# Performance work log

Hardware: AMD Instinct MI355X
Metric: run time of the kernel (lower is better)

Reference implementation:

```python
import jax, jax.numpy as jnp
import numpy as np

EPS = 1e-6
HID = 2048; N_HEADS = 16; Q_LORA = 768; KV_LORA = 512
ROPE_D = 64; NOPE_D = 128; V_D = 128
IDX_H = 32; IDX_D = 128; IDX_TOPK = 512
N_EXP = 8; TOPK = 4; N_GROUP = 4; TOPK_GROUP = 2
MOE_I = 512; SHARED_I = 512; ROUTED_SCALE = 2.5
T = 1024
NEG = -1e30


def _rms(x, w, eps=EPS):
    x = x.astype(jnp.float32)
    return x * jax.lax.rsqrt(jnp.mean(x * x, axis=-1, keepdims=True) + eps) * w


def _ln(x, w, b, eps=EPS):
    x = x.astype(jnp.float32)
    m = jnp.mean(x, axis=-1, keepdims=True)
    v = jnp.mean((x - m) ** 2, axis=-1, keepdims=True)
    return (x - m) * jax.lax.rsqrt(v + eps) * w + b


def _rope_cs(positions, dim):
    inv = 1.0 / (10000.0 ** (jnp.arange(0, dim, 2, dtype=jnp.float32) / dim))
    f = positions.astype(jnp.float32)[:, None] * inv[None, :]  # [T, dim/2]
    return jnp.cos(f), jnp.sin(f)


def _rope(x, cos, sin):
    # neox-style rotate-half over last dim
    d = x.shape[-1] // 2
    x1, x2 = x[..., :d], x[..., d:]
    while cos.ndim < x.ndim:
        cos, sin = cos[:, None], sin[:, None]
    return jnp.concatenate([x1 * cos - x2 * sin, x2 * cos + x1 * sin], axis=-1)


def setup_inputs() -> dict:
    key = jax.random.key(0)
    ks = iter(jax.random.split(key, 32))
    w = lambda *s: jax.random.normal(next(ks), s, jnp.float32) * 0.02
    inp = {
        'positions': jnp.arange(T, dtype=jnp.int32),
        'hidden_states': jax.random.normal(next(ks), (T, HID), jnp.float32),
        'residual': jax.random.normal(next(ks), (T, HID), jnp.float32),
        'w_input_ln': jnp.ones((HID,), jnp.float32),
        'w_post_ln': jnp.ones((HID,), jnp.float32),
        'w_step1': w(Q_LORA + KV_LORA + ROPE_D + IDX_D + IDX_H, HID),
        'w_q_a_ln': jnp.ones((Q_LORA,), jnp.float32),
        'w_kv_a_ln': jnp.ones((KV_LORA,), jnp.float32),
        'idx_k_ln_w': jnp.ones((IDX_D,), jnp.float32),
        'idx_k_ln_b': jnp.zeros((IDX_D,), jnp.float32),
        'w_step3': w(IDX_H * IDX_D + N_HEADS * (NOPE_D + ROPE_D), Q_LORA),
        'W_UK_T': w(N_HEADS, NOPE_D, KV_LORA),
        'W_UV': w(N_HEADS, KV_LORA, V_D),
        'w_o': w(HID, N_HEADS * V_D),
        'gate_w': w(N_EXP, HID),
        'gate_bias': jnp.zeros((N_EXP,), jnp.float32),
        'shared_gate_up': w(2 * SHARED_I, HID),
        'shared_down': w(HID, SHARED_I),
        'exp_gate_up': w(N_EXP, 2 * MOE_I, HID),
        'exp_down': w(N_EXP, HID, MOE_I),
    }
    return inp


def reference(positions, hidden_states, residual, w_input_ln, w_post_ln, w_step1,
              w_q_a_ln, w_kv_a_ln, idx_k_ln_w, idx_k_ln_b, w_step3, W_UK_T, W_UV,
              w_o, gate_w, gate_bias, shared_gate_up, shared_down, exp_gate_up, exp_down):
    Tn = hidden_states.shape[0]
    rows = jnp.arange(Tn)
    # (allreduce is identity at tp=1) + residual add + RMSNorm
    res = hidden_states.astype(jnp.float32) + residual.astype(jnp.float32)
    h = _rms(res, w_input_ln)
    # ---- Step 1: fused qkv_a + indexer_wk + indexer_weights_proj GEMM ----
    s1 = h @ w_step1.T
    o0 = 0
    q_c = s1[:, o0:o0 + Q_LORA]; o0 += Q_LORA
    kv_c = s1[:, o0:o0 + KV_LORA]; o0 += KV_LORA
    k_pe = s1[:, o0:o0 + ROPE_D]; o0 += ROPE_D
    idx_k = s1[:, o0:o0 + IDX_D]; o0 += IDX_D
    idx_w_raw = s1[:, o0:o0 + IDX_H]
    cos, sin = _rope_cs(positions, ROPE_D)
    # fused_norm_rope: norms + rope on k_pe / indexer-k
    q_c = _rms(q_c, w_q_a_ln)
    kv_c = _rms(kv_c, w_kv_a_ln)
    k_pe = _rope(k_pe, cos, sin)
    idx_k = _ln(idx_k, idx_k_ln_w, idx_k_ln_b)
    idx_k = jnp.concatenate([_rope(idx_k[:, :ROPE_D], cos, sin), idx_k[:, ROPE_D:]], axis=-1)
    # ---- Step 3: fused indexer_wq_b + q_b_proj GEMM ----
    s3 = q_c @ w_step3.T
    idx_q = s3[:, :IDX_H * IDX_D].reshape(Tn, IDX_H, IDX_D)
    q = s3[:, IDX_H * IDX_D:].reshape(Tn, N_HEADS, NOPE_D + ROPE_D)
    q_nope, q_pe = q[..., :NOPE_D], q[..., NOPE_D:]
    # absorb W_UK: [T,H,nope] x [H,nope,kv_lora] -> [T,H,kv_lora]
    ql_nope = jnp.einsum('thn,hnk->thk', q_nope, W_UK_T)
    q_pe = _rope(q_pe, cos, sin)
    idx_q = jnp.concatenate([_rope(idx_q[..., :ROPE_D], cos, sin), idx_q[..., ROPE_D:]], axis=-1)
    idx_q = idx_q * (IDX_D ** -0.5)            # indexer softmax scale
    idx_w = idx_w_raw * (IDX_H ** -0.5)        # per-head weights scale
    # ---- sparse attention indexer: relu(q.k) head-weighted sum, causal top-k ----
    il = jnp.einsum('thd,sd->ths', idx_q, idx_k)          # [T,Hi,S]
    iscores = jnp.einsum('ths,th->ts', jax.nn.relu(il), idx_w)
    causal = positions[:, None] >= positions[None, :]
    iscores = jnp.where(causal, iscores, NEG)
    topk_idx = jax.lax.top_k(iscores, IDX_TOPK)[1]        # [T, IDX_TOPK]
    tmask = jnp.zeros((Tn, Tn), bool).at[rows[:, None], topk_idx].set(True)
    mask = causal & tmask
    # ---- MLA MQA attention in latent space ----
    mqa_q = jnp.concatenate([ql_nope, jnp.broadcast_to(q_pe, (Tn, N_HEADS, ROPE_D))], axis=-1)
    kv = jnp.concatenate([kv_c, k_pe], axis=-1)           # [S, kv_lora+rope]
    att = jnp.einsum('thd,sd->hts', mqa_q, kv) * ((NOPE_D + ROPE_D) ** -0.5)
    att = jnp.where(mask[None], att, NEG)
    p = jax.nn.softmax(att, axis=-1)
    o = jnp.einsum('hts,sk->thk', p, kv_c)                # [T,H,kv_lora]
    o = jnp.einsum('thk,hkv->thv', o, W_UV).reshape(Tn, N_HEADS * V_D)
    attn_out = o @ w_o.T
    # add + RMSNorm
    res2 = attn_out + res
    h2 = _rms(res2, w_post_ln)
    # ---- MoE: DeepSeekV3 sigmoid grouped routing + shared experts ----
    glog = h2 @ gate_w.T
    sg = jax.nn.sigmoid(glog)
    sc = sg + gate_bias
    gsz = N_EXP // N_GROUP
    grp = sc.reshape(Tn, N_GROUP, gsz)
    grp_score = jax.lax.top_k(grp, min(2, gsz))[0].sum(-1)
    gidx = jax.lax.top_k(grp_score, TOPK_GROUP)[1]
    gmask = jnp.zeros((Tn, N_GROUP), bool).at[rows[:, None], gidx].set(True)
    emask = jnp.repeat(gmask, gsz, axis=1)
    sc_m = jnp.where(emask, sc, NEG)
    _, tid = jax.lax.top_k(sc_m, TOPK)
    tw = jnp.take_along_axis(sg, tid, axis=1)
    tw = tw / (tw.sum(-1, keepdims=True) + 1e-20) * ROUTED_SCALE
    comb = jnp.zeros((Tn, N_EXP), jnp.float32).at[rows[:, None], tid].set(tw)
    # routed experts (dense masked combine as reference for grouped-GEMM dispatch)
    gu = jnp.einsum('th,eih->tei', h2, exp_gate_up)       # [T,E,2I]
    act = jax.nn.silu(gu[..., :MOE_I]) * gu[..., MOE_I:]
    routed_e = jnp.einsum('tei,ehi->teh', act, exp_down)  # [T,E,H]
    routed = jnp.einsum('te,teh->th', comb, routed_e)
    # shared experts
    gus = h2 @ shared_gate_up.T
    shared = (jax.nn.silu(gus[:, :SHARED_I]) * gus[:, SHARED_I:]) @ shared_down.T
    out = shared + routed
    return out, res2
```

## Files before the change

### kernel.cpp

```cpp
#include <hip/hip_runtime.h>
#include <math.h>

static constexpr int TT  = 1024;
static constexpr int HID = 2048;
static constexpr int NH  = 16;
static constexpr int QL  = 768;
static constexpr int KVL = 512;
static constexpr int RD  = 64;
static constexpr int IH  = 32;
static constexpr int ID  = 128;
static constexpr int S1W = QL + KVL + RD + ID + IH;
static constexpr int S3W = IH*ID + NH*(128+RD);

#define SCALE_ATT 0.07216878364870323f
#define SC_IDXQ   0.08838834764831845f
#define SC_IDXW   0.17677669529663687f
#define NEGR      -1e30f
#define NEGL      -3.0e38f

typedef __bf16 bf16x8 __attribute__((ext_vector_type(8)));
typedef float  f32x4  __attribute__((ext_vector_type(4)));

#define GLD_LDS16(g, l) __builtin_amdgcn_global_load_lds( \
    (const __attribute__((address_space(1))) void*)(g),   \
    (__attribute__((address_space(3))) void*)(l), 16, 0, 0)

__device__ __forceinline__ unsigned short f2b(float x) {
  union { float f; unsigned u; } v; v.f = x;
  unsigned r = v.u + 0x7FFFu + ((v.u >> 16) & 1u);
  return (unsigned short)(r >> 16);
}
__device__ __forceinline__ float b2f(unsigned short u) {
  union { unsigned u; float f; } v; v.u = ((unsigned)u) << 16;
  return v.f;
}

__device__ __forceinline__ float blk_sum256(float v, float* s) {
  #pragma unroll
  for (int o = 32; o > 0; o >>= 1) v += __shfl_down(v, o, 64);
  __syncthreads();
  if ((threadIdx.x & 63) == 0) s[threadIdx.x >> 6] = v;
  __syncthreads();
  return s[0] + s[1] + s[2] + s[3];
}

__global__ __launch_bounds__(256) void k_prelude(const float* __restrict__ hs,
                                                 const float* __restrict__ rsd,
                                                 const float* __restrict__ w,
                                                 float* __restrict__ res,
                                                 unsigned short* __restrict__ hb) {
  int t = blockIdx.x;
  __shared__ float scr[4];
  float vals[8]; float ss = 0.f;
  #pragma unroll
  for (int r = 0; r < 8; r++) {
    int d = threadIdx.x + 256*r;
    float v = hs[(size_t)t*HID + d] + rsd[(size_t)t*HID + d];
    vals[r] = v; res[(size_t)t*HID + d] = v; ss = fmaf(v, v, ss);
  }
  ss = blk_sum256(ss, scr);
  float inv = 1.f/sqrtf(ss/(float)HID + 1e-6f);
  #pragma unroll
  for (int r = 0; r < 8; r++) {
    int d = threadIdx.x + 256*r;
    hb[(size_t)t*HID + d] = f2b(vals[r]*inv*w[d]);
  }
}

__global__ __launch_bounds__(256) void k_res2(const float* __restrict__ attn1,
                                              const float* __restrict__ attn2,
                                              const float* __restrict__ res,
                                              const float* __restrict__ w,
                                              float* __restrict__ res2_out,
                                              float* __restrict__ h2,
                                              unsigned short* __restrict__ h2b) {
  int t = blockIdx.x;
  __shared__ float scr[4];
  float vals[8]; float ss = 0.f;
  #pragma unroll
  for (int r = 0; r < 8; r++) {
    int d = threadIdx.x + 256*r;
    float v = attn1[(size_t)t*HID + d] + attn2[(size_t)t*HID + d] + res[(size_t)t*HID + d];
    vals[r] = v; res2_out[(size_t)t*HID + d] = v; ss = fmaf(v, v, ss);
  }
  ss = blk_sum256(ss, scr);
  float inv = 1.f/sqrtf(ss/(float)HID + 1e-6f);
  #pragma unroll
  for (int r = 0; r < 8; r++) {
    int d = threadIdx.x + 256*r;
    float o = vals[r]*inv*w[d];
    h2[(size_t)t*HID + d] = o;
    h2b[(size_t)t*HID + d] = f2b(o);
  }
}

__global__ void k_ropecs(const int* __restrict__ pos, float* __restrict__ cosb, float* __restrict__ sinb) {
  int i = blockIdx.x*256 + threadIdx.x;
  if (i >= TT*32) return;
  int t = i >> 5, k = i & 31;
  double inv = pow(10000.0, -((double)(2*k))/64.0);
  double f = (double)pos[t] * inv;
  cosb[i] = (float)cos(f);
  sinb[i] = (float)sin(f);
}

__global__ void k_f2b(const float* __restrict__ s, unsigned short* __restrict__ d,
                      long long n, long long ntot) {
  long long stride = (long long)gridDim.x * 1024;
  for (long long i = ((long long)blockIdx.x*256 + threadIdx.x)*4; i < ntot; i += stride) {
    float x0, x1, x2, x3;
    if (i + 3 < n) { float4 v = *(const float4*)(s + i); x0=v.x; x1=v.y; x2=v.z; x3=v.w; }
    else {
      x0 = (i   < n) ? s[i]   : 0.f; x1 = (i+1 < n) ? s[i+1] : 0.f;
      x2 = (i+2 < n) ? s[i+2] : 0.f; x3 = (i+3 < n) ? s[i+3] : 0.f;
    }
    ushort4 o; o.x=f2b(x0); o.y=f2b(x1); o.z=f2b(x2); o.w=f2b(x3);
    *(ushort4*)(d + i) = o;
  }
}

__global__ void k_f2b4(const float* __restrict__ s0, unsigned short* __restrict__ d0, long long n0,
                       const float* __restrict__ s1, unsigned short* __restrict__ d1, long long n1,
                       const float* __restrict__ s2, unsigned short* __restrict__ d2, long long n2,
                       const float* __restrict__ s3, unsigned short* __restrict__ d3, long long n3) {
  long long ntot = n0 + n1 + n2 + n3;
  long long stride = (long long)gridDim.x * 1024;
  for (long long i = ((long long)blockIdx.x*256 + threadIdx.x)*4; i < ntot; i += stride) {
    const float* s; unsigned short* d; long long j = i;
    if (j < n0) { s = s0; d = d0; }
    else { j -= n0;
      if (j < n1) { s = s1; d = d1; }
      else { j -= n1;
        if (j < n2) { s = s2; d = d2; }
        else { j -= n2; s = s3; d = d3; } } }
    float4 v = *(const float4*)(s + j);
    ushort4 o; o.x=f2b(v.x); o.y=f2b(v.y); o.z=f2b(v.z); o.w=f2b(v.w);
    *(ushort4*)(d + j) = o;
  }
}

__global__ __launch_bounds__(256) void k_tconvb(const float* __restrict__ src,
                                                unsigned short* __restrict__ dst,
                                                int R, int C) {
  src += (size_t)blockIdx.z * R * C;
  dst += (size_t)blockIdx.z * R * C;
  __shared__ float tile[32][33];
  int c0 = blockIdx.x * 32, r0 = blockIdx.y * 32;
  int tx = threadIdx.x & 31, ty = threadIdx.x >> 5;
  #pragma unroll
  for (int i = 0; i < 4; i++) {
    int r = r0 + ty + i*8;
    tile[ty + i*8][tx] = src[(size_t)r*C + c0 + tx];
  }
  __syncthreads();
  #pragma unroll
  for (int i = 0; i < 4; i++) {
    int c = c0 + ty + i*8;
    dst[(size_t)c*R + r0 + tx] = f2b(tile[tx][ty + i*8]);
  }
}

template<int OUT, bool ILV, int MOE>
__global__ __launch_bounds__(256) void k_mgemm(
    const unsigned short* __restrict__ A, int lda, long long sA,
    const unsigned short* __restrict__ B, int ldb, long long sB,
    void* __restrict__ Cv, int ldc, long long sC,
    int N, int K, float alpha, int cskip, int ktri,
    int nseg, long long segA, long long segB,
    const float* __restrict__ comb,
    const int* __restrict__ cntp, const int* __restrict__ tokp) {
  const int row0 = blockIdx.y * 128;
  const int col0 = blockIdx.x * 128;
  if (cskip >= 0 && col0 > row0 + cskip) return;
  const int zb = blockIdx.z;
  int cnt = 0; long long off = 0;
  if (MOE) {
    cnt = cntp[zb];
    for (int e = 0; e < zb; e++) off += cntp[e];
    if (row0 >= cnt) return;
  }
  __shared__ __align__(16) unsigned short As[128*64];
  __shared__ __align__(16) unsigned short Bs[128*64];
  const int tid  = threadIdx.x;
  const int wave = tid >> 6, lane = tid & 63;
  const int wm = wave >> 1, wn = wave & 1;
  A += (size_t)zb * (size_t)sA;
  B += (size_t)zb * (size_t)sB;
  if (MOE == 2) A += off * (long long)lda;

  int tki[4];
  if (MOE == 1) {
    #pragma unroll
    for (int it = 0; it < 4; it++) {
      int r = (wave*64 + it*256 + lane) >> 3;
      tki[it] = tokp[zb*1024 + row0 + r];
    }
  }

  f32x4 acc[4][4] = {};
  const int l15 = lane & 15, l4 = lane >> 4;
  const int sx = l15 & 7;
  const int Kend = (ktri && K > row0 + 128) ? (row0 + 128) : K;

  for (int seg = 0; seg < nseg; seg++) {
    const unsigned short* Ab = A + (size_t)seg * segA;
    const unsigned short* Bb = B + (size_t)seg * segB;
    for (int k0 = 0; k0 < Kend; k0 += 64) {
      __syncthreads();
      #pragma unroll
      for (int it = 0; it < 4; it++) {
        int base = wave*64 + it*256;
        int sidx = base + lane;
        int r = sidx >> 3, s = sidx & 7;
        int s_src = s ^ (r & 7);
        const unsigned short* ga;
        if (MOE == 1) ga = Ab + (size_t)tki[it]*lda + k0 + s_src*8;
        else          ga = Ab + (size_t)(row0 + r)*lda + k0 + s_src*8;
        GLD_LDS16(ga, As + base*8);
        int rt = col0 + r;
        int srow = ILV ? ((rt >> 1) + (rt & 1)*512) : rt;
        const unsigned short* gb = Bb + (size_t)srow*ldb + k0 + s_src*8;
        GLD_LDS16(gb, Bs + base*8);
      }
      __syncthreads();
      #pragma unroll
      for (int kc = 0; kc < 2; kc++) {
        const int sl = ((kc*4 + l4) ^ sx) << 3;
        bf16x8 fa[4], fb[4];
        #pragma unroll
        for (int mf = 0; mf < 4; mf++)
          fa[mf] = *(const bf16x8*)&As[(wm*64 + mf*16 + l15)*64 + sl];
        #pragma unroll
        for (int nf = 0; nf < 4; nf++)
          fb[nf] = *(const bf16x8*)&Bs[(wn*64 + nf*16 + l15)*64 + sl];
        #pragma unroll
        for (int mf = 0; mf < 4; mf++)
          #pragma unroll
          for (int nf = 0; nf < 4; nf++)
            acc[mf][nf] = __builtin_amdgcn_mfma_f32_16x16x32_bf16(fa[mf], fb[nf], acc[mf][nf], 0, 0, 0);
      }
    }
  }

  #pragma unroll
  for (int mf = 0; mf < 4; mf++) {
    #pragma unroll
    for (int nf = 0; nf < 4; nf++) {
      int n = col0 + wn*64 + nf*16 + l15;
      #pragma unroll
      for (int r = 0; r < 4; r++) {
        int m = row0 + wm*64 + mf*16 + l4*4 + r;
        float v = acc[mf][nf][r] * alpha;
        if (OUT == 2) {
          float p = __shfl_xor(v, 1, 64);
          if ((l15 & 1) == 0) {
            bool ok = true;
            long long mrow = m;
            float w;
            if (MOE == 1) {
              ok = (m < cnt); mrow = off + m;
              int tok = tokp[zb*1024 + m];
              w = (zb < 8) ? comb[tok*8 + zb] : 1.f;
            } else {
              w = (zb < 8) ? comb[m*8 + zb] : 1.f;
            }
            if (ok) {
              float rres = v/(1.f + expf(-v)) * p * w;
              ((unsigned short*)Cv)[(size_t)zb*sC + (size_t)mrow*ldc + (n >> 1)] = f2b(rres);
            }
          }
        } else if (n < N) {
          bool ok = true;
          long long mrow = m;
          if (MOE == 2) { ok = (m < cnt); mrow = off + m; }
          if (ok) {
            size_t idx = (size_t)mrow*ldc + n;
            if (OUT == 1) ((unsigned short*)Cv)[(size_t)zb*sC + idx] = f2b(v);
            else          ((float*)Cv)[(size_t)zb*sC + idx] = v;
          }
        }
      }
    }
  }
}

__global__ __launch_bounds__(256) void k_post1(const float* __restrict__ s1a,
    const float* __restrict__ s1b,
    const float* __restrict__ wq, const float* __restrict__ wkv,
    const float* __restrict__ lnw, const float* __restrict__ lnb,
    const float* __restrict__ cosb, const float* __restrict__ sinb,
    unsigned short* __restrict__ qcb, float* __restrict__ kvc, float* __restrict__ kpe,
    float* __restrict__ idxk, float* __restrict__ idxw) {
  int t = blockIdx.x, tid = threadIdx.x;
  __shared__ float rowb[S1W];
  __shared__ float scr[4];
  __shared__ float yb[128];
  for (int d = tid; d < S1W; d += 256)
    rowb[d] = s1a[(size_t)t*S1W + d] + s1b[(size_t)t*S1W + d];
  __syncthreads();
  float ss = 0.f;
  for (int d = tid; d < QL; d += 256) { float v = rowb[d]; ss = fmaf(v,v,ss); }
  ss = blk_sum256(ss, scr);
  float inv = 1.f/sqrtf(ss/(float)QL + 1e-6f);
  for (int d = tid; d < QL; d += 256) qcb[(size_t)t*QL + d] = f2b(rowb[d]*inv*wq[d]);
  ss = 0.f;
  for (int d = tid; d < KVL; d += 256) { float v = rowb[QL+d]; ss = fmaf(v,v,ss); }
  ss = blk_sum256(ss, scr);
  inv = 1.f/sqrtf(ss/(float)KVL + 1e-6f);
  for (int d = tid; d < KVL; d += 256) kvc[(size_t)t*KVL + d] = rowb[QL+d]*inv*wkv[d];
  float sm = (tid < 128) ? rowb[1344 + tid] : 0.f;
  float tot = blk_sum256(sm, scr);
  float mean = tot / 128.f;
  float vs = 0.f;
  if (tid < 128) { float v = rowb[1344+tid] - mean; vs = v*v; }
  vs = blk_sum256(vs, scr);
  float ivn = 1.f/sqrtf(vs/128.f + 1e-6f);
  if (tid < 128) yb[tid] = (rowb[1344+tid]-mean)*ivn*lnw[tid] + lnb[tid];
  __syncthreads();
  if (tid < 32) {
    float c = cosb[t*32 + tid], s = sinb[t*32 + tid];
    idxk[(size_t)t*ID + tid]      = yb[tid]*c - yb[32+tid]*s;
    idxk[(size_t)t*ID + 32 + tid] = yb[32+tid]*c + yb[tid]*s;
    float x1 = rowb[1280+tid], x2 = rowb[1312+tid];
    kpe[(size_t)t*RD + tid]      = x1*c - x2*s;
    kpe[(size_t)t*RD + 32 + tid] = x2*c + x1*s;
    idxw[(size_t)t*IH + tid] = rowb[1472+tid] * SC_IDXW;
  } else if (tid >= 64 && tid < 128) {
    idxk[(size_t)t*ID + tid] = yb[tid];
  }
}

__global__ __launch_bounds__(256) void k_post3b(const float* __restrict__ s3,
                                                const float* __restrict__ cosb,
                                                const float* __restrict__ sinb,
                                                unsigned short* __restrict__ s3b) {
  int t = blockIdx.x, tid = threadIdx.x;
  const float* row = s3 + (size_t)t*S3W;
  __shared__ float buf[S3W];
  __shared__ float cs[32], sn[32];
  if (tid < 32) { cs[tid] = cosb[t*32+tid]; sn[tid] = sinb[t*32+tid]; }
  for (int d = tid; d < S3W; d += 256) buf[d] = row[d];
  __syncthreads();
  for (int p = tid; p < 1024; p += 256) {
    int h = p >> 5, d = p & 31;
    float c = cs[d], s = sn[d];
    float x1 = buf[h*ID + d], x2 = buf[h*ID + 32 + d];
    buf[h*ID + d]      = (x1*c - x2*s) * SC_IDXQ;
    buf[h*ID + 32 + d] = (x2*c + x1*s) * SC_IDXQ;
  }
  for (int p = tid; p < 2048; p += 256) {
    int h = p >> 6, d = 64 + (p & 63);
    buf[h*ID + d] *= SC_IDXQ;
  }
  for (int p = tid; p < 512; p += 256) {
    int h = p >> 5, d = p & 31;
    float c = cs[d], s = sn[d];
    int base = IH*ID + h*192 + 128;
    float x1 = buf[base + d], x2 = buf[base + 32 + d];
    buf[base + d]      = x1*c - x2*s;
    buf[base + 32 + d] = x2*c + x1*s;
  }
  __syncthreads();
  unsigned short* orow = s3b + (size_t)t*S3W;
  for (int g = tid*4; g < S3W; g += 1024) {
    ushort4 o;
    o.x = f2b(buf[g]); o.y = f2b(buf[g+1]); o.z = f2b(buf[g+2]); o.w = f2b(buf[g+3]);
    *(ushort4*)(orow + g) = o;
  }
}

__global__ void k_qpe(const unsigned short* __restrict__ s3b, unsigned short* __restrict__ qm) {
  int i = blockIdx.x*256 + threadIdx.x;
  int t = i >> 10, r = i & 1023;
  int h = r >> 6, j = r & 63;
  float v = b2f(s3b[(size_t)t*S3W + IH*ID + h*192 + 128 + j]) * SCALE_ATT;
  qm[(size_t)t*9216 + h*576 + 512 + j] = f2b(v);
}

__global__ void k_kvb(const float* __restrict__ kvc, const float* __restrict__ kpe,
                      unsigned short* __restrict__ kvb) {
  int i = blockIdx.x*256 + threadIdx.x;
  int s = i / 576, d = i - s*576;
  float v = (d < 512) ? kvc[(size_t)s*KVL + d] : kpe[(size_t)s*RD + (d - 512)];
  kvb[i] = f2b(v);
}

__global__ __launch_bounds__(256) void k_ired(const float* __restrict__ il,
                                              const float* __restrict__ idxw,
                                              float* __restrict__ isc,
                                              int first, int last, int h0) {
  int tr = blockIdx.x;
  int t = 512 + tr;
  int s0 = threadIdx.x * 4;
  float4 acc;
  if (first) acc = make_float4(0.f, 0.f, 0.f, 0.f);
  else       acc = *(float4*)(isc + (size_t)tr*TT + s0);
  #pragma unroll
  for (int hh = 0; hh < 8; hh++) {
    float w = idxw[t*IH + h0 + hh];
    float4 v = *(const float4*)(il + (size_t)hh*524288 + (size_t)tr*1024 + s0);
    acc.x += fmaxf(v.x, 0.f) * w;
    acc.y += fmaxf(v.y, 0.f) * w;
    acc.z += fmaxf(v.z, 0.f) * w;
    acc.w += fmaxf(v.w, 0.f) * w;
  }
  if (last) {
    if (s0     > t) acc.x = NEGR;
    if (s0 + 1 > t) acc.y = NEGR;
    if (s0 + 2 > t) acc.z = NEGR;
    if (s0 + 3 > t) acc.w = NEGR;
  }
  *(float4*)(isc + (size_t)tr*TT + s0) = acc;
}

__global__ __launch_bounds__(512) void k_topk(const float* __restrict__ isc,
                                              unsigned char* __restrict__ mask) {
  int t = 512 + blockIdx.x;
  const float* row = isc + (size_t)blockIdx.x * TT;
  __shared__ unsigned long long keys[1024];
  int tid = threadIdx.x;
  for (int i = tid; i < 1024; i += 512) {
    float v = row[i];
    unsigned int b = __float_as_uint(v);
    unsigned int u = (b & 0x80000000u) ? ~b : (b | 0x80000000u);
    keys[i] = ((unsigned long long)u << 32) | (unsigned int)(1023 - i);
  }
  __syncthreads();
  for (int k = 2; k <= 1024; k <<= 1) {
    for (int j = k >> 1; j > 0; j >>= 1) {
      int i = ((tid & ~(j - 1)) << 1) | (tid & (j - 1));
      int l = i | j;
      unsigned long long a = keys[i], b = keys[l];
      bool up = ((i & k) == 0);
      if ((a < b) == up) { keys[i] = b; keys[l] = a; }
      __syncthreads();
    }
  }
  unsigned char* mrow = mask + (size_t)t * TT;
  for (int p = tid; p < 1024; p += 512) {
    int s = 1023 - (int)(keys[p] & 0xFFFFFFFFu);
    mrow[s] = (p < 512) ? (unsigned char)1 : (unsigned char)0;
  }
}

__global__ __launch_bounds__(256) void k_psoft(unsigned short* __restrict__ pb,
                                               const unsigned char* __restrict__ mask) {
  int b = blockIdx.x;
  int t = b & 1023, h = b >> 10;
  unsigned short* row = pb + ((size_t)h << 20) + ((size_t)t << 10);
  int tid = threadIdx.x;
  __shared__ float scr[4];
  int s0 = tid * 4;
  int rub = ((t >> 7) + 1) << 7;
  bool act = (s0 < rub);
  float v0 = 0.f, v1 = 0.f, v2 = 0.f, v3 = 0.f;
  bool m0 = false, m1 = false, m2 = false, m3 = false;
  if (act) {
    ushort4 raw = *(const ushort4*)(row + s0);
    v0 = b2f(raw.x); v1 = b2f(raw.y); v2 = b2f(raw.z); v3 = b2f(raw.w);
    if (t < 512) {
      m0 = (s0 <= t); m1 = (s0+1 <= t); m2 = (s0+2 <= t); m3 = (s0+3 <= t);
    } else {
      uchar4 mk = *(const uchar4*)(mask + (size_t)t*TT + s0);
      m0 = (s0 <= t) && mk.x; m1 = (s0+1 <= t) && mk.y;
      m2 = (s0+2 <= t) && mk.z; m3 = (s0+3 <= t) && mk.w;
    }
  }
  float mx = NEGL;
  if (m0) mx = v0;
  if (m1) mx = fmaxf(mx, v1);
  if (m2) mx = fmaxf(mx, v2);
  if (m3) mx = fmaxf(mx, v3);
  #pragma unroll
  for (int o = 32; o > 0; o >>= 1) mx = fmaxf(mx, __shfl_down(mx, o, 64));
  __syncthreads();
  if ((tid & 63) == 0) scr[tid >> 6] = mx;
  __syncthreads();
  mx = fmaxf(fmaxf(scr[0], scr[1]), fmaxf(scr[2], scr[3]));
  float p0 = m0 ? expf(v0 - mx) : 0.f;
  float p1 = m1 ? expf(v1 - mx) : 0.f;
  float p2 = m2 ? expf(v2 - mx) : 0.f;
  float p3 = m3 ? expf(v3 - mx) : 0.f;
  float sum = blk_sum256((p0+p1)+(p2+p3), scr);
  float inv = 1.f / sum;
  if (act) {
    ushort4 o;
    o.x = f2b(p0*inv); o.y = f2b(p1*inv); o.z = f2b(p2*inv); o.w = f2b(p3*inv);
    *(ushort4*)(row + s0) = o;
  }
}

__global__ __launch_bounds__(256) void k_gate(const float* __restrict__ h2,
                                              const float* __restrict__ gw,
                                              const float* __restrict__ gb,
                                              float* __restrict__ comb) {
  int t = blockIdx.x, tid = threadIdx.x;
  int e = tid >> 5, lane = tid & 31;
  __shared__ float gl[8];
  float p = 0.f;
  for (int d = lane; d < HID; d += 32) p = fmaf(h2[(size_t)t*HID+d], gw[(size_t)e*HID+d], p);
  #pragma unroll
  for (int o = 16; o > 0; o >>= 1) p += __shfl_down(p, o, 32);
  if (lane == 0) gl[e] = p;
  __syncthreads();
  if (tid == 0) {
    float sg[8], sc[8];
    #pragma unroll
    for (int i = 0; i < 8; i++) { sg[i] = 1.f/(1.f+expf(-gl[i])); sc[i] = sg[i] + gb[i]; }
    float gs[4];
    #pragma unroll
    for (int g = 0; g < 4; g++) gs[g] = sc[2*g] + sc[2*g+1];
    int g0 = 0;
    for (int g = 1; g < 4; g++) if (gs[g] > gs[g0]) g0 = g;
    int g1 = -1;
    for (int g = 0; g < 4; g++) { if (g == g0) continue; if (g1 < 0 || gs[g] > gs[g1]) g1 = g; }
    float wsum = 1e-20f;
    #pragma unroll
    for (int i = 0; i < 8; i++) { int g = i >> 1; if (g == g0 || g == g1) wsum += sg[i]; }
    #pragma unroll
    for (int i = 0; i < 8; i++) { int g = i >> 1; comb[t*8+i] = (g == g0 || g == g1) ? sg[i]/wsum*2.5f : 0.f; }
  }
}

__global__ __launch_bounds__(1024) void k_route(const float* __restrict__ comb,
                                                int* __restrict__ tokidx,
                                                int* __restrict__ rank,
                                                int* __restrict__ cntp) {
  int e = blockIdx.x;
  int t = threadIdx.x;
  if (e == 8) {
    tokidx[8*1024 + t] = t;
    if (t == 0) cntp[8] = 1024;
    return;
  }
  int lane = t & 63, w = t >> 6;
  bool sel = comb[t*8 + e] != 0.0f;
  unsigned long long bal = __ballot(sel);
  int pw = __popcll(bal & ((1ull << lane) - 1ull));
  int wt = __popcll(bal);
  __shared__ int wsum[16];
  if (lane == 0) wsum[w] = wt;
  __syncthreads();
  int woff = 0, total = 0;
  #pragma unroll
  for (int i = 0; i < 16; i++) { int v = wsum[i]; if (i < w) woff += v; total += v; }
  int pos = woff + pw;
  rank[t*8 + e] = sel ? pos : -1;
  if (sel) tokidx[e*1024 + pos] = t;
  __syncthreads();
  if (t >= total) tokidx[e*1024 + t] = 0;
  if (t == 0) cntp[e] = total;
}

__global__ __launch_bounds__(256) void k_rsum(const float* __restrict__ dpc,
                                              const int* __restrict__ rank,
                                              const int* __restrict__ cntp,
                                              float* __restrict__ out) {
  int t = blockIdx.x;
  int d = threadIdx.x * 8;
  int offs[8]; int acc_off = 0;
  #pragma unroll
  for (int e = 0; e < 8; e++) { offs[e] = acc_off; acc_off += cntp[e]; }
  const float* ps = dpc + (size_t)(acc_off + t)*2048 + d;
  float4 a0 = *(const float4*)ps;
  float4 a1 = *(const float4*)(ps + 4);
  #pragma unroll
  for (int e = 0; e < 8; e++) {
    int r = rank[t*8 + e];
    if (r >= 0) {
      const float* p = dpc + (size_t)(offs[e] + r)*2048 + d;
      float4 b0 = *(const float4*)p;
      float4 b1 = *(const float4*)(p + 4);
      a0.x += b0.x; a0.y += b0.y; a0.z += b0.z; a0.w += b0.w;
      a1.x += b1.x; a1.y += b1.y; a1.z += b1.z; a1.w += b1.w;
    }
  }
  float* po = out + (size_t)t*2048 + d;
  *(float4*)po = a0;
  *(float4*)(po + 4) = a1;
}

extern "C" void kernel_launch(void* const* d_in, const int* in_sizes, int n_in,
                              void* d_out, int out_size, void* d_ws, size_t ws_size,
                              hipStream_t stream) {
  const int*   positions = (const int*)d_in[0];
  const float* hs     = (const float*)d_in[1];
  const float* rsd    = (const float*)d_in[2];
  const float* w_in   = (const float*)d_in[3];
  const float* w_post = (const float*)d_in[4];
  const float* w_s1   = (const float*)d_in[5];
  const float* w_qln  = (const float*)d_in[6];
  const float* w_kvln = (const float*)d_in[7];
  const float* iklnw  = (const float*)d_in[8];
  const float* iklnb  = (const float*)d_in[9];
  const float* w_s3   = (const float*)d_in[10];
  const float* wukt   = (const float*)d_in[11];
  const float* wuv    = (const float*)d_in[12];
  const float* w_o    = (const float*)d_in[13];
  const float* gate_w = (const float*)d_in[14];
  const float* gate_b = (const float*)d_in[15];
  const float* sh_gu  = (const float*)d_in[16];
  const float* sh_dn  = (const float*)d_in[17];
  const float* ex_gu  = (const float*)d_in[18];
  const float* ex_dn  = (const float*)d_in[19];

  float* ws = (float*)d_ws;
  typedef unsigned short ush;
  float* RES   = ws + 0;
  float* COSB  = ws + 2097152;
  float* SINB  = ws + 2129920;
  float* KVC   = ws + 2162688;
  float* KPE   = ws + 2686976;
  float* IDXK  = ws + 2752512;
  float* IDXW  = ws + 2883584;
  float* COMB  = ws + 2916352;
  ush*   HB    = (ush*)(ws + 2924544);
  ush*   WS1B  = (ush*)(ws + 3973120);
  float* S1P0  = ws + 5545984;
  ush*   QCB   = (ush*)(ws + 7086080);
  ush*   WS3B  = (ush*)(ws + 7479296);
  ush*   WOB   = (ush*)(ws + 7479296);
  float* S3    = ws + 10231808;
  float* S1P1  = ws + 10231808;
  ush*   S3B   = (ush*)(ws + 17571840);
  ush*   WUKTB = (ush*)(ws + 21241856);
  ush*   QMQAB = (ush*)(ws + 21766144);
  float* ISC   = ws + 26484736;
  unsigned char* MASK = (unsigned char*)(ws + 27009024);
  ush*   WUVB  = (ush*)(ws + 27271168);
  ush*   KVB   = (ush*)(ws + 27795456);
  ush*   VTB   = (ush*)(ws + 28090368);
  ush*   O2B   = (ush*)(ws + 28352512);
  float* ILB   = ws + 27795456;
  ush*   IDXKB = (ush*)(ws + 31989760);
  ush*   PB    = (ush*)(ws + 10231808);
  ush*   OHB   = (ush*)(ws + 18620416);
  float* ATTNP = ws + 10231808;
  float* H2     = ws + 2924544;
  ush*   H2B    = (ush*)(ws + 5021696);
  ush*   EXGUB  = (ush*)(ws + 6070272);
  ush*   SHGUB  = (ush*)(ws + 14458880);
  ush*   EXDNB  = (ush*)(ws + 15507456);
  ush*   SHDNB  = (ush*)(ws + 19701760);
  ush*   ACTC   = (ush*)(ws + 20226048);
  float* DPC    = ws + 21536768;
  int*   TOKIDX = (int*)(ws + 32022528);
  int*   RANK   = (int*)(ws + 32031744);
  int*   CNT    = (int*)(ws + 32039936);

  float* OUT0 = (float*)d_out;
  float* OUT_RES2 = OUT0 + (size_t)TT*HID;

  k_prelude<<<TT, 256, 0, stream>>>(hs, rsd, w_in, RES, HB);
  k_ropecs<<<(TT*32)/256, 256, 0, stream>>>(positions, COSB, SINB);
  k_f2b<<<1024, 256, 0, stream>>>(w_s1, WS1B, 3080192LL, 3145728LL);
  k_f2b<<<1024, 256, 0, stream>>>(w_s3, WS3B, 5505024LL, 5505024LL);
  k_tconvb<<<dim3(16,4,16), 256, 0, stream>>>(wukt, WUKTB, 128, 512);
  k_tconvb<<<dim3(4,16,16), 256, 0, stream>>>(wuv, WUVB, 512, 128);
  k_mgemm<0,false,0><<<dim3(12,8,2), 256, 0, stream>>>(
      HB, 2048, 1024, WS1B, 2048, 1024, S1P0, S1W, 4685824,
      1504, 1024, 1.f, -1, 0, 1, 0, 0, nullptr, nullptr, nullptr);
  k_post1<<<TT, 256, 0, stream>>>(S1P0, S1P1, w_qln, w_kvln, iklnw, iklnb, COSB, SINB, QCB, KVC, KPE, IDXK, IDXW);
  k_f2b<<<128, 256, 0, stream>>>(IDXK, IDXKB, 131072LL, 131072LL);
  k_mgemm<0,false,0><<<dim3(56,8,1), 256, 0, stream>>>(
      QCB, 768, 0, WS3B, 768, 0, S3, S3W, 0,
      S3W, 768, 1.f, -1, 0, 1, 0, 0, nullptr, nullptr, nullptr);
  k_post3b<<<TT, 256, 0, stream>>>(S3, COSB, SINB, (ush*)S3B);
  k_f2b<<<1024, 256, 0, stream>>>(w_o, WOB, 4194304LL, 4194304LL);
  k_mgemm<1,false,0><<<dim3(4,8,16), 256, 0, stream>>>(
      S3B + 4096, S3W, 192, WUKTB, 128, 65536, QMQAB, 9216, 576,
      512, 128, SCALE_ATT, -1, 0, 1, 0, 0, nullptr, nullptr, nullptr);
  k_qpe<<<4096, 256, 0, stream>>>(S3B, QMQAB);
  for (int c = 0; c < 4; c++) {
    k_mgemm<0,false,0><<<dim3(8,4,8), 256, 0, stream>>>(
        S3B + (size_t)512*S3W + c*1024, S3W, 128, IDXKB, 128, 0,
        ILB, 1024, 524288, 1024, 128, 1.f, 639, 0, 1, 0, 0, nullptr, nullptr, nullptr);
    k_ired<<<512, 256, 0, stream>>>(ILB, IDXW, ISC, c == 0, c == 3, c*8);
  }
  k_topk<<<512, 512, 0, stream>>>(ISC, MASK);
  k_kvb<<<2304, 256, 0, stream>>>(KVC, KPE, KVB);
  k_tconvb<<<dim3(16,32,1), 256, 0, stream>>>(KVC, VTB, 1024, 512);
  k_mgemm<1,false,0><<<dim3(8,8,16), 256, 0, stream>>>(
      QMQAB, 9216, 576, KVB, 576, 0, PB, 1024, 1048576,
      1024, 576, 1.f, 127, 0, 1, 0, 0, nullptr, nullptr, nullptr);
  k_psoft<<<16384, 256, 0, stream>>>(PB, MASK);
  k_mgemm<1,false,0><<<dim3(4,8,16), 256, 0, stream>>>(
      PB, 1024, 1048576, VTB, 1024, 0, OHB, 512, 524288,
      512, 1024, 1.f, -1, 1, 1, 0, 0, nullptr, nullptr, nullptr);
  k_mgemm<1,false,0><<<dim3(1,8,16), 256, 0, stream>>>(
      OHB, 512, 524288, WUVB, 512, 65536, O2B, 2048, 128,
      128, 512, 1.f, -1, 0, 1, 0, 0, nullptr, nullptr, nullptr);
  k_mgemm<0,false,0><<<dim3(16,8,2), 256, 0, stream>>>(
      O2B, 2048, 1024, WOB, 2048, 1024, ATTNP, 2048, 2097152,
      2048, 1024, 1.f, -1, 0, 1, 0, 0, nullptr, nullptr, nullptr);
  k_res2<<<TT, 256, 0, stream>>>(ATTNP, ATTNP + 2097152, RES, w_post, OUT_RES2, H2, H2B);
  k_gate<<<TT, 256, 0, stream>>>(H2, gate_w, gate_b, COMB);
  k_route<<<9, 1024, 0, stream>>>(COMB, TOKIDX, RANK, CNT);
  k_f2b4<<<2048, 256, 0, stream>>>(ex_gu, EXGUB, 16777216LL,
                                   sh_gu, SHGUB, 2097152LL,
                                   ex_dn, EXDNB, 8388608LL,
                                   sh_dn, SHDNB, 1048576LL);
  k_mgemm<2,true,1><<<dim3(8,8,9), 256, 0, stream>>>(
      H2B, 2048, 0, EXGUB, 2048, 2097152, ACTC, 512, 0,
      1024, 2048, 1.f, -1, 0, 1, 0, 0, COMB, CNT, TOKIDX);
  k_mgemm<0,false,2><<<dim3(16,8,9), 256, 0, stream>>>(
      ACTC, 512, 0, EXDNB, 512, 1048576, DPC, 2048, 0,
      2048, 512, 1.f, -1, 0, 1, 0, 0, nullptr, CNT, nullptr);
  k_rsum<<<TT, 256, 0, stream>>>(DPC, RANK, CNT, OUT0);
}
```

Baseline: 454.0 us.

## Double-buffer LDS tiles in generic MFMA GEMM to overlap loads with compute

Shared memory for the A and B tiles is doubled so the next K-tile (across segments) is prefetched via global_load_lds while MFMAs consume the current buffer. The segment and K loops are flattened into one tile loop with a single barrier per iteration. This aims to hide global load latency behind compute, at the cost of doubled LDS use (64KB per block), which may reduce occupancy.

Result: faster. 424.8 us (-6.4%).

```diff
diff --git a/kernel.cpp b/kernel.cpp
--- a/kernel.cpp
+++ b/kernel.cpp
@@ -179,8 +179,8 @@
     for (int e = 0; e < zb; e++) off += cntp[e];
     if (row0 >= cnt) return;
   }
-  __shared__ __align__(16) unsigned short As[128*64];
-  __shared__ __align__(16) unsigned short Bs[128*64];
+  __shared__ __align__(16) unsigned short As[2][128*64];
+  __shared__ __align__(16) unsigned short Bs[2][128*64];
   const int tid  = threadIdx.x;
   const int wave = tid >> 6, lane = tid & 63;
   const int wm = wave >> 1, wn = wave & 1;
@@ -201,45 +201,57 @@
   const int l15 = lane & 15, l4 = lane >> 4;
   const int sx = l15 & 7;
   const int Kend = (ktri && K > row0 + 128) ? (row0 + 128) : K;
-
-  for (int seg = 0; seg < nseg; seg++) {
-    const unsigned short* Ab = A + (size_t)seg * segA;
-    const unsigned short* Bb = B + (size_t)seg * segB;
-    for (int k0 = 0; k0 < Kend; k0 += 64) {
-      __syncthreads();
+  const int nk = Kend >> 6;
+  const int nt = nseg * nk;
+
+  auto STAGE = [&](int b, const unsigned short* Ab, const unsigned short* Bb, int k0) {
+    #pragma unroll
+    for (int it = 0; it < 4; it++) {
+      int base = wave*64 + it*256;
+      int sidx = base + lane;
+      int r = sidx >> 3, s = sidx & 7;
+      int s_src = s ^ (r & 7);
+      const unsigned short* ga;
+      if (MOE == 1) ga = Ab + (size_t)tki[it]*lda + k0 + s_src*8;
+      else          ga = Ab + (size_t)(row0 + r)*lda + k0 + s_src*8;
+      GLD_LDS16(ga, &As[b][base*8]);
+      int rt = col0 + r;
+      int srow = ILV ? ((rt >> 1) + (rt & 1)*512) : rt;
+      const unsigned short* gb = Bb + (size_t)srow*ldb + k0 + s_src*8;
+      GLD_LDS16(gb, &Bs[b][base*8]);
+    }
+  };
+
+  STAGE(0, A, B, 0);
+  int ks = 64, sg = 0;
+  if (ks == Kend) { ks = 0; sg = 1; }
+  __syncthreads();
+  int cur = 0;
+
+  for (int u = 0; u < nt; u++) {
+    if (u + 1 < nt) {
+      STAGE(cur ^ 1, A + (size_t)sg*segA, B + (size_t)sg*segB, ks);
+      ks += 64;
+      if (ks == Kend) { ks = 0; sg++; }
+    }
+    #pragma unroll
+    for (int kc = 0; kc < 2; kc++) {
+      const int sl = ((kc*4 + l4) ^ sx) << 3;
+      bf16x8 fa[4], fb[4];
       #pragma unroll
-      for (int it = 0; it < 4; it++) {
-        int base = wave*64 + it*256;
-        int sidx = base + lane;
-        int r = sidx >> 3, s = sidx & 7;
-        int s_src = s ^ (r & 7);
-        const unsigned short* ga;
-        if (MOE == 1) ga = Ab + (size_t)tki[it]*lda + k0 + s_src*8;
-        else          ga = Ab + (size_t)(row0 + r)*lda + k0 + s_src*8;
-        GLD_LDS16(ga, As + base*8);
-        int rt = col0 + r;
-        int srow = ILV ? ((rt >> 1) + (rt & 1)*512) : rt;
-        const unsigned short* gb = Bb + (size_t)srow*ldb + k0 + s_src*8;
-        GLD_LDS16(gb, Bs + base*8);
-      }
-      __syncthreads();
+      for (int mf = 0; mf < 4; mf++)
+        fa[mf] = *(const bf16x8*)&As[cur][(wm*64 + mf*16 + l15)*64 + sl];
       #pragma unroll
-      for (int kc = 0; kc < 2; kc++) {
-        const int sl = ((kc*4 + l4) ^ sx) << 3;
-        bf16x8 fa[4], fb[4];
-        #pragma unroll
-        for (int mf = 0; mf < 4; mf++)
-          fa[mf] = *(const bf16x8*)&As[(wm*64 + mf*16 + l15)*64 + sl];
+      for (int nf = 0; nf < 4; nf++)
+        fb[nf] = *(const bf16x8*)&Bs[cur][(wn*64 + nf*16 + l15)*64 + sl];
+      #pragma unroll
+      for (int mf = 0; mf < 4; mf++)
         #pragma unroll
         for (int nf = 0; nf < 4; nf++)
-          fb[nf] = *(const bf16x8*)&Bs[(wn*64 + nf*16 + l15)*64 + sl];
-        #pragma unroll
-        for (int mf = 0; mf < 4; mf++)
-          #pragma unroll
-          for (int nf = 0; nf < 4; nf++)
-            acc[mf][nf] = __builtin_amdgcn_mfma_f32_16x16x32_bf16(fa[mf], fb[nf], acc[mf][nf], 0, 0, 0);
-      }
-    }
+          acc[mf][nf] = __builtin_amdgcn_mfma_f32_16x16x32_bf16(fa[mf], fb[nf], acc[mf][nf], 0, 0, 0);
+    }
+    __syncthreads();
+    cur ^= 1;
   }
 
   #pragma unroll
```
